# Performance work log

Measured on AMD Instinct MI355X. Metric: run time of the kernel, lower is better.

The kernel has to match this reference:

```python
import jax, jax.numpy as jnp
import numpy as np

# pywt db4 decomposition filters (dec_lo / dec_hi), exactly as pywt.Wavelet('db4')
DEC_LO = np.array([-0.010597401784997278, 0.032883011666982945, 0.030841381835986965,
                   -0.18703481171888114, -0.02798376941698385, 0.6308807679295904,
                   0.7148465705525415, 0.23037781330885523], dtype=np.float32)
DEC_HI = np.array([-0.23037781330885523, 0.7148465705525415, -0.6308807679295904,
                   -0.02798376941698385, 0.18703481171888114, 0.030841381835986965,
                   -0.032883011666982945, -0.010597401784997278], dtype=np.float32)

PATCH_LEN, STRIDE, PAD = 8, 4, 4


def _dwt(x, lo_rev, hi_rev):
    """Single-level pywt dwt with mode='symmetric' along last axis.
    pywt: out[i] = sum_j h[j] * x_ext[2i+1-j]  ->  correlate reversed filter
    with symmetric-extended signal starting at offset 1."""
    F = lo_rev.shape[0]  # 8
    n = x.shape[-1]
    out_len = (n + F - 1) // 2
    ext = jnp.pad(x, [(0, 0)] * (x.ndim - 1) + [(F - 1, F - 1)], mode='symmetric')
    # window index matrix: (out_len, F), windows start at 1, 3, 5, ...
    idx = 1 + 2 * np.arange(out_len)[:, None] + np.arange(F)[None, :]
    win = ext[..., idx]                      # (..., out_len, F)
    return win @ lo_rev, win @ hi_rev        # (cA, cD)


def setup_inputs() -> dict:
    key = jax.random.key(0)
    k1, k2 = jax.random.split(key)
    B, C, T, V = 32, 3, 4096, 25
    x = jax.random.normal(k1, (B, C, T, V), dtype=jnp.float32)
    # nn.Linear(in=C*28, out=128, bias=False) weight, (out, in) layout
    W = jax.random.normal(k2, (128, C * 28), dtype=jnp.float32) * (1.0 / np.sqrt(C * 28))
    return {"x": x, "W": W}


def reference(x, W):
    B, C, T, V = x.shape
    # ReplicationPad2d((0,0,0,PAD)) pads end of time axis (dim -2) by edge replication
    xp = jnp.pad(x, ((0, 0), (0, 0), (0, PAD), (0, 0)), mode='edge')
    P = (T + PAD - PATCH_LEN) // STRIDE + 1
    widx = STRIDE * np.arange(P)[:, None] + np.arange(PATCH_LEN)  # (P, L)
    xw = xp[:, :, widx, :]                   # (B, C, P, L, V)
    xw = xw.transpose(0, 4, 2, 1, 3)         # (B, V, P, C, L) == torch permute(0,3,2,1,4)

    lo_rev = jnp.asarray(DEC_LO[::-1].copy())
    hi_rev = jnp.asarray(DEC_HI[::-1].copy())
    cA, cD = _dwt(xw, lo_rev, hi_rev)        # each (B, V, P, C, 7)
    aa, ad = _dwt(cA, lo_rev, hi_rev)        # level-2 nodes of approx
    da, dd = _dwt(cD, lo_rev, hi_rev)        # level-2 nodes of detail
    y = jnp.concatenate([aa, ad, dd, da], axis=-1)  # (B, V, P, C, 28)
    y = y.reshape(B, V * P, C * 28)
    return y @ W.T                           # (B, V*P, 128)
```

## Files before the change

kernel.cpp:

```cpp
#include <hip/hip_runtime.h>
#include <hip/hip_bf16.h>

struct M28x8 { float m[28][8]; };

constexpr double DLO[8] = {-0.010597401784997278, 0.032883011666982945,
                            0.030841381835986965, -0.18703481171888114,
                           -0.02798376941698385,   0.6308807679295904,
                            0.7148465705525415,    0.23037781330885523};
constexpr double DHI[8] = {-0.23037781330885523,   0.7148465705525415,
                           -0.6308807679295904,   -0.02798376941698385,
                            0.18703481171888114,   0.030841381835986965,
                           -0.032883011666982945, -0.010597401784997278};

constexpr void dwt_c(const double* x, int n, double* lo, double* hi) {
    int out_len = (n + 7) / 2;
    for (int i = 0; i < out_len; ++i) {
        double a = 0.0, d = 0.0;
        for (int j = 0; j < 8; ++j) {
            int q = 2 * i + j - 6;
            if (q < 0) q = -q - 1;
            if (q >= n) q = 2 * n - 1 - q;
            a += DLO[7 - j] * x[q];
            d += DHI[7 - j] * x[q];
        }
        lo[i] = a; hi[i] = d;
    }
}

constexpr M28x8 build_M() {
    M28x8 R{};
    for (int j = 0; j < 8; ++j) {
        double x[8] = {0,0,0,0,0,0,0,0};
        x[j] = 1.0;
        double cA[7] = {}, cD[7] = {};
        dwt_c(x, 8, cA, cD);
        double aa[7] = {}, ad[7] = {}, da[7] = {}, dd[7] = {};
        dwt_c(cA, 7, aa, ad);
        dwt_c(cD, 7, da, dd);
        for (int i = 0; i < 7; ++i) {
            R.m[i][j]      = (float)aa[i];
            R.m[7 + i][j]  = (float)ad[i];
            R.m[14 + i][j] = (float)dd[i];
            R.m[21 + i][j] = (float)da[i];
        }
    }
    return R;
}

__constant__ M28x8 g_M = build_M();

__global__ void wfold_kernel(const float* __restrict__ W, float* __restrict__ Wf) {
    int t = blockIdx.x * blockDim.x + threadIdx.x;
    if (t >= 128 * 24) return;
    int o = t / 24;
    int cj = t - o * 24;
    int c = cj >> 3;
    int j = cj & 7;
    const float* wr = W + o * 84 + c * 28;
    float acc = 0.f;
#pragma unroll
    for (int k = 0; k < 28; ++k) acc += wr[k] * g_M.m[k][j];
    Wf[t] = acc;
}

#define PT   16
#define TT   (4 * PT + 4)
#define SLAB (3 * 25 * TT)

__global__ __launch_bounds__(256) void wave_kernel(const float* __restrict__ x,
                                                   const float* __restrict__ Wf,
                                                   float* __restrict__ out) {
    __shared__ float s_x[SLAB];
    const int tile = blockIdx.x;
    const int b    = blockIdx.y;
    const int t0   = tile * (4 * PT);
    const int tid  = threadIdx.x;

    for (int lin = tid; lin < SLAB; lin += 256) {
        int v  = lin % 25;
        int r  = lin / 25;
        int tt = r % TT;
        int c  = r / TT;
        int t  = t0 + tt;
        if (t > 4095) t = 4095;
        s_x[(c * 25 + v) * TT + tt] = x[((b * 3 + c) * 4096 + t) * 25 + v];
    }

    const int o = tid & 127;
    const int s = tid >> 7;
    float w[24];
#pragma unroll
    for (int q = 0; q < 6; ++q) {
        float4 f = ((const float4*)(Wf + o * 24))[q];
        w[4 * q + 0] = f.x; w[4 * q + 1] = f.y;
        w[4 * q + 2] = f.z; w[4 * q + 3] = f.w;
    }

    __syncthreads();

    const int out_base = (b * 25600 + tile * PT) * 128 + o;
    for (int idx = s; idx < 25 * PT; idx += 2) {
        int v  = idx >> 4;
        int pl = idx & 15;
        float acc = 0.f;
#pragma unroll
        for (int c = 0; c < 3; ++c) {
            const float4* row = (const float4*)(s_x + (c * 25 + v) * TT + 4 * pl);
            float4 a = row[0];
            float4 bq = row[1];
            acc += w[c*8+0]*a.x  + w[c*8+1]*a.y  + w[c*8+2]*a.z  + w[c*8+3]*a.w
                 + w[c*8+4]*bq.x + w[c*8+5]*bq.y + w[c*8+6]*bq.z + w[c*8+7]*bq.w;
        }
        out[out_base + (v * 1024 + pl) * 128] = acc;
    }
}

extern "C" void kernel_launch(void* const* d_in, const int* in_sizes, int n_in,
                              void* d_out, int out_size, void* d_ws, size_t ws_size,
                              hipStream_t stream) {
    const float* x = (const float*)d_in[0];
    const float* W = (const float*)d_in[1];
    float* out = (float*)d_out;
    float* Wf  = (float*)d_ws;

    hipLaunchKernelGGL(wfold_kernel, dim3(12), dim3(256), 0, stream, W, Wf);
    hipLaunchKernelGGL(wave_kernel, dim3(64, 32), dim3(256), 0, stream, x, Wf, out);
}
```

Measured before the change: 485.7 us.

## Register-block four output channels per thread with vectorized float4 stores

Each thread now computes four adjacent output channels instead of one, reusing each pair of LDS x reads across four weight rows held in registers. Results are written with a single float4 store per thread, and eight 32-thread groups stride over the patch/vertex rows. This cuts LDS traffic per output and widens global stores, at the cost of much higher register use (96 weight values), with launch bounds set to keep two blocks per CU.

```diff
diff --git a/kernel.cpp b/kernel.cpp
--- a/kernel.cpp
+++ b/kernel.cpp
@@ -67,9 +67,9 @@
 #define TT   (4 * PT + 4)
 #define SLAB (3 * 25 * TT)
 
-__global__ __launch_bounds__(256) void wave_kernel(const float* __restrict__ x,
-                                                   const float* __restrict__ Wf,
-                                                   float* __restrict__ out) {
+__global__ __launch_bounds__(256, 2) void wave_kernel(const float* __restrict__ x,
+                                                      const float* __restrict__ Wf,
+                                                      float* __restrict__ out) {
     __shared__ float s_x[SLAB];
     const int tile = blockIdx.x;
     const int b    = blockIdx.y;
@@ -86,32 +86,44 @@
         s_x[(c * 25 + v) * TT + tt] = x[((b * 3 + c) * 4096 + t) * 25 + v];
     }
 
-    const int o = tid & 127;
-    const int s = tid >> 7;
-    float w[24];
+    const int og  = tid & 31;
+    const int grp = tid >> 5;
+    const int o   = og << 2;
+
+    float wr[4][24];
 #pragma unroll
-    for (int q = 0; q < 6; ++q) {
-        float4 f = ((const float4*)(Wf + o * 24))[q];
-        w[4 * q + 0] = f.x; w[4 * q + 1] = f.y;
-        w[4 * q + 2] = f.z; w[4 * q + 3] = f.w;
+    for (int m = 0; m < 4; ++m) {
+        const float4* wp = (const float4*)(Wf + (o + m) * 24);
+#pragma unroll
+        for (int q = 0; q < 6; ++q) {
+            float4 f = wp[q];
+            wr[m][4 * q + 0] = f.x; wr[m][4 * q + 1] = f.y;
+            wr[m][4 * q + 2] = f.z; wr[m][4 * q + 3] = f.w;
+        }
     }
 
     __syncthreads();
 
-    const int out_base = (b * 25600 + tile * PT) * 128 + o;
-    for (int idx = s; idx < 25 * PT; idx += 2) {
-        int v  = idx >> 4;
-        int pl = idx & 15;
-        float acc = 0.f;
+    const long out_blk = (long)(b * 25600 + tile * PT) * 128 + o;
+    for (int idx = grp; idx < 25 * PT; idx += 8) {
+        const int v  = idx >> 4;
+        const int pl = idx & 15;
+        float acc[4] = {0.f, 0.f, 0.f, 0.f};
 #pragma unroll
         for (int c = 0; c < 3; ++c) {
             const float4* row = (const float4*)(s_x + (c * 25 + v) * TT + 4 * pl);
-            float4 a = row[0];
-            float4 bq = row[1];
-            acc += w[c*8+0]*a.x  + w[c*8+1]*a.y  + w[c*8+2]*a.z  + w[c*8+3]*a.w
-                 + w[c*8+4]*bq.x + w[c*8+5]*bq.y + w[c*8+6]*bq.z + w[c*8+7]*bq.w;
+            float4 xa = row[0];
+            float4 xb = row[1];
+#pragma unroll
+            for (int m = 0; m < 4; ++m) {
+                acc[m] += wr[m][c*8+0]*xa.x + wr[m][c*8+1]*xa.y
+                        + wr[m][c*8+2]*xa.z + wr[m][c*8+3]*xa.w
+                        + wr[m][c*8+4]*xb.x + wr[m][c*8+5]*xb.y
+                        + wr[m][c*8+6]*xb.z + wr[m][c*8+7]*xb.w;
+            }
         }
-        out[out_base + (v * 1024 + pl) * 128] = acc;
+        float4 st = {acc[0], acc[1], acc[2], acc[3]};
+        *(float4*)(out + out_blk + (long)(v * 1024 + pl) * 128) = st;
     }
 }
 
```

Result: faster. 460.3 us (-5.2%).
